# Optimization experiments

Hardware: AMD Instinct MI355X
Metric: run time of the kernel (lower is better)

## Reference

```python
import jax, jax.numpy as jnp
import numpy as np

N, E, M = 100000, 3200000, 1000000  # nodes, message edges, scored move edges
DIN, H = 128, 64


def setup_inputs() -> dict:
    key = jax.random.key(0)
    ks = jax.random.split(key, 20)
    rn = lambda k, shape, s=0.05: (jax.random.normal(k, shape, jnp.float32) * s)
    return {
        "x": jax.random.normal(ks[0], (N, DIN), jnp.float32),
        "edge_index": jax.random.randint(ks[1], (2, E), 0, N, jnp.int64),
        "move_edge_index": jax.random.randint(ks[2], (2, M), 0, N, jnp.int64),
        "lin1_w": rn(ks[3], (DIN, H)), "lin1_b": jnp.zeros((H,), jnp.float32),
        "lin2_w": rn(ks[4], (H, H)), "lin2_b": jnp.zeros((H,), jnp.float32),
        "conv1_wl": rn(ks[5], (H, H)), "conv1_bl": jnp.zeros((H,), jnp.float32),
        "conv1_wr": rn(ks[6], (H, H)),
        "conv2_wl": rn(ks[7], (H, H)), "conv2_bl": jnp.zeros((H,), jnp.float32),
        "conv2_wr": rn(ks[8], (H, H)),
        "mlp_w1": rn(ks[9], (2 * H, H)), "mlp_b1": jnp.zeros((H,), jnp.float32),
        "mlp_w2": rn(ks[10], (H, 1)), "mlp_b2": jnp.zeros((1,), jnp.float32),
    }


def reference(x, edge_index, move_edge_index,
              lin1_w, lin1_b, lin2_w, lin2_b,
              conv1_wl, conv1_bl, conv1_wr,
              conv2_wl, conv2_bl, conv2_wr,
              mlp_w1, mlp_b1, mlp_w2, mlp_b2):
    n = x.shape[0]
    src, dst = edge_index[0], edge_index[1]
    # mean-aggregation degrees (PyG SAGEConv default aggr='mean'; isolated nodes -> 0)
    deg = jax.ops.segment_sum(jnp.ones(src.shape, x.dtype), dst, num_segments=n)
    inv_deg = (jnp.where(deg > 0, 1.0 / jnp.maximum(deg, 1.0), 0.0))[:, None]

    def sage(h, wl, bl, wr):
        # out = W_l @ mean_j h_j + b_l + W_r @ h_i
        agg = jax.ops.segment_sum(h[src], dst, num_segments=n) * inv_deg
        return agg @ wl + bl + h @ wr

    h = jax.nn.relu(x @ lin1_w + lin1_b)
    h = jax.nn.relu(sage(h, conv1_wl, conv1_bl, conv1_wr))
    h = jax.nn.relu(h @ lin2_w + lin2_b)
    h = jax.nn.relu(sage(h, conv2_wl, conv2_bl, conv2_wr))

    # edge scoring: gather src/dst embeddings, concat, 2-layer MLP, tanh
    cat = jnp.concatenate([h[move_edge_index[0]], h[move_edge_index[1]]], axis=1)  # [M, 2H]
    logits = (jax.nn.relu(cat @ mlp_w1 + mlp_b1) @ mlp_w2 + mlp_b2).reshape(-1)
    return jnp.tanh(logits)
```

## Files before the change

### kernel.cpp

```cpp
#include <hip/hip_runtime.h>
#include <math.h>

#define MAXB 512
#define PART_BS 1024
#define NBLK_MAX 248
#define CAPB 96

typedef _Float16 f16;
typedef __attribute__((ext_vector_type(2))) _Float16 f16x2;
typedef __attribute__((ext_vector_type(4))) _Float16 f16x4;
typedef __attribute__((ext_vector_type(8))) _Float16 f16x8;
typedef __attribute__((ext_vector_type(4))) float f32x4;

static __device__ __forceinline__ unsigned short f2h(float f) {
    f16 h = (f16)f; return *(unsigned short*)&h;
}

__global__ __launch_bounds__(PART_BS) void k_part(const int* __restrict__ src,
                                                  const int* __restrict__ dst,
                                                  unsigned* __restrict__ bb,
                                                  int* __restrict__ cnt,
                                                  int E, int shift, int pcap,
                                                  int nblk, int nb) {
    __shared__ int h[MAXB];
    const int blk = blockIdx.x;
    const int b0 = blk * pcap;
    const int e1 = min(b0 + pcap, E);
    for (int i = threadIdx.x; i < MAXB; i += PART_BS) h[i] = 0;
    __syncthreads();
    const unsigned mask = (1u << shift) - 1u;
    for (int pos = b0 + (int)threadIdx.x * 8; pos < e1; pos += PART_BS * 8) {
        if (pos + 8 <= e1) {
            int4 d0 = *(const int4*)(dst + pos), d1 = *(const int4*)(dst + pos + 4);
            int4 s0 = *(const int4*)(src + pos), s1 = *(const int4*)(src + pos + 4);
            int dd[8] = {d0.x, d0.y, d0.z, d0.w, d1.x, d1.y, d1.z, d1.w};
            int ss[8] = {s0.x, s0.y, s0.z, s0.w, s1.x, s1.y, s1.z, s1.w};
#pragma unroll
            for (int k = 0; k < 8; ++k) {
                int b = dd[k] >> shift;
                int r = atomicAdd(&h[b], 1);
                if (r < CAPB)
                    bb[((size_t)b * nblk + blk) * CAPB + r] =
                        ((unsigned)ss[k] << shift) | ((unsigned)dd[k] & mask);
            }
        } else {
            for (int k = 0; pos + k < e1; ++k) {
                int d = dst[pos + k];
                int b = d >> shift;
                int r = atomicAdd(&h[b], 1);
                if (r < CAPB)
                    bb[((size_t)b * nblk + blk) * CAPB + r] =
                        ((unsigned)src[pos + k] << shift) | ((unsigned)d & mask);
            }
        }
    }
    __syncthreads();
    for (int i = threadIdx.x; i < nb; i += PART_BS)
        cnt[(size_t)i * nblk + blk] = min(h[i], CAPB);
}

__global__ __launch_bounds__(512) void k_bfill(const unsigned* __restrict__ bb,
                                               const int* __restrict__ cnt,
                                               int* __restrict__ row_st,
                                               int* __restrict__ row_en,
                                               float* __restrict__ inv_deg,
                                               int* __restrict__ csr,
                                               int N, int shift, int CAP, int nblk) {
    __shared__ int deg[512], cur[512], s[512];
    __shared__ int scnt[NBLK_MAX];
    int b = blockIdx.x;
    int t = threadIdx.x;
    int lo = b << shift;
    int hi = min(N, (b + 1) << shift);
    int nn = hi - lo;
    unsigned off = (unsigned)b * CAP;
    unsigned mask = (1u << shift) - 1u;
    const unsigned* seg = bb + (size_t)b * nblk * CAPB;

    for (int i = t; i < nblk; i += 512) scnt[i] = cnt[(size_t)b * nblk + i];
    deg[t] = 0;
    __syncthreads();
    const int tot8 = (nblk * CAPB) >> 3;
    for (int q8 = t; q8 < tot8; q8 += 512) {
        int i = q8 << 3;
        int si = i / CAPB;
        int r = i - si * CAPB;
        int sc = scnt[si];
        if (r < sc) {
            uint4 wA = *(const uint4*)&seg[i];
            uint4 wB = *(const uint4*)&seg[i + 4];
            int nv = min(sc - r, 8);
            unsigned ww[8] = {wA.x, wA.y, wA.z, wA.w, wB.x, wB.y, wB.z, wB.w};
#pragma unroll
            for (int k = 0; k < 8; ++k)
                if (k < nv) atomicAdd(&deg[ww[k] & mask], 1);
        }
    }
    __syncthreads();
    int d = deg[t];
    int pd = (d + 31) & ~31;
    s[t] = pd;
    __syncthreads();
    for (int o = 1; o < 512; o <<= 1) {
        int u = (t >= o) ? s[t - o] : 0;
        __syncthreads();
        s[t] += u;
        __syncthreads();
    }
    int excl = min(s[t] - pd, CAP);
    int pe = min(excl + pd, CAP);
    cur[t] = excl;
    if (t < nn) {
        row_st[lo + t] = (int)off + excl;
        row_en[lo + t] = (int)off + pe;
        inv_deg[lo + t] = d > 0 ? 1.0f / (float)d : 0.0f;
        for (int j = excl + d; j < pe; ++j) csr[off + j] = N;
    }
    __syncthreads();
    for (int q8 = t; q8 < tot8; q8 += 512) {
        int i = q8 << 3;
        int si = i / CAPB;
        int r = i - si * CAPB;
        int sc = scnt[si];
        if (r < sc) {
            uint4 wA = *(const uint4*)&seg[i];
            uint4 wB = *(const uint4*)&seg[i + 4];
            int nv = min(sc - r, 8);
            unsigned ww[8] = {wA.x, wA.y, wA.z, wA.w, wB.x, wB.y, wB.z, wB.w};
#pragma unroll
            for (int k = 0; k < 8; ++k)
                if (k < nv) {
                    int dl = (int)(ww[k] & mask);
                    int pos = atomicAdd(&cur[dl], 1);
                    if (pos < CAP) csr[off + pos] = (int)(ww[k] >> shift);
                }
        }
    }
}

__global__ __launch_bounds__(256) void k_prep(
    const float* __restrict__ lin1_w, const float* __restrict__ c1_wl,
    const float* __restrict__ c1_wr, const float* __restrict__ lin2_w,
    const float* __restrict__ c2_wl, const float* __restrict__ c2_wr,
    const float* __restrict__ mlp_w1, const float* __restrict__ mlp_w2,
    unsigned short* __restrict__ Wt) {
    int i = blockIdx.x * 256 + threadIdx.x;
    for (; i < 36928; i += gridDim.x * 256) {
        float v;
        if (i < 8192)       { int j = i;         int n = j >> 7, k = j & 127; v = lin1_w[k * 64 + n]; }
        else if (i < 16384) { int j = i - 8192;  int n = j >> 7, k = j & 127;
                              v = (k < 64) ? c1_wl[k * 64 + n] : c1_wr[(k - 64) * 64 + n]; }
        else if (i < 20480) { int j = i - 16384; int n = j >> 6, k = j & 63;  v = lin2_w[k * 64 + n]; }
        else if (i < 28672) { int j = i - 20480; int n = j >> 7, k = j & 127;
                              v = (k < 64) ? c2_wl[k * 64 + n] : c2_wr[(k - 64) * 64 + n]; }
        else if (i < 32768) { int j = i - 28672; int n = j >> 6, k = j & 63;  v = mlp_w1[k * 64 + n]; }
        else if (i < 36864) { int j = i - 32768; int n = j >> 6, k = j & 63;  v = mlp_w1[(k + 64) * 64 + n]; }
        else                { v = mlp_w2[i - 36864]; }
        Wt[i] = f2h(v);
    }
}

__global__ __launch_bounds__(256) void k_gather_h(
    const _Float16* __restrict__ hh, const int* __restrict__ csr,
    const int* __restrict__ row_st, const int* __restrict__ row_en,
    const float* __restrict__ inv_deg, _Float16* __restrict__ out, int n) {
    int node = (blockIdx.x * 256 + (int)threadIdx.x) >> 6;
    if (node >= n) return;
    int lane = threadIdx.x & 63;
    int g = lane >> 3, sub = lane & 7;
    int base = row_st[node], end = row_en[node];
    float a[8] = {0.f, 0.f, 0.f, 0.f, 0.f, 0.f, 0.f, 0.f};
#if __has_builtin(__builtin_amdgcn_fdot2)
    const f16x2 one2 = {(f16)1.f, (f16)1.f};
#endif
    for (; base + 64 <= end; base += 64) {
        int4 sA = *(const int4*)&csr[base + 4 * g];
        int4 sB = *(const int4*)&csr[base + 32 + 4 * g];
        int sidx[8] = {sA.x, sA.y, sA.z, sA.w, sB.x, sB.y, sB.z, sB.w};
        f16x8 u[8];
#pragma unroll
        for (int t = 0; t < 8; ++t)
            u[t] = *(const f16x8*)(hh + (((unsigned)sidx[t] << 6) + ((unsigned)sub << 3)));
#if __has_builtin(__builtin_amdgcn_fdot2)
#pragma unroll
        for (int t = 0; t < 8; t += 2)
#pragma unroll
            for (int j = 0; j < 8; ++j) {
                f16x2 v = {u[t][j], u[t + 1][j]};
                a[j] = __builtin_amdgcn_fdot2(v, one2, a[j], false);
            }
#else
#pragma unroll
        for (int t = 0; t < 8; ++t)
#pragma unroll
            for (int j = 0; j < 8; ++j) a[j] += (float)u[t][j];
#endif
    }
    if (base < end) {
        int4 sA = *(const int4*)&csr[base + 4 * g];
        int sidx[4] = {sA.x, sA.y, sA.z, sA.w};
        f16x8 u[4];
#pragma unroll
        for (int t = 0; t < 4; ++t)
            u[t] = *(const f16x8*)(hh + (((unsigned)sidx[t] << 6) + ((unsigned)sub << 3)));
#if __has_builtin(__builtin_amdgcn_fdot2)
#pragma unroll
        for (int t = 0; t < 4; t += 2)
#pragma unroll
            for (int j = 0; j < 8; ++j) {
                f16x2 v = {u[t][j], u[t + 1][j]};
                a[j] = __builtin_amdgcn_fdot2(v, one2, a[j], false);
            }
#else
#pragma unroll
        for (int t = 0; t < 4; ++t)
#pragma unroll
            for (int j = 0; j < 8; ++j) a[j] += (float)u[t][j];
#endif
    }
#pragma unroll
    for (int j = 0; j < 8; ++j) {
        a[j] += __shfl_xor(a[j], 8, 64);
        a[j] += __shfl_xor(a[j], 16, 64);
        a[j] += __shfl_xor(a[j], 32, 64);
    }
    if (g == 0) {
        float idv = inv_deg[node];
        f16x8 o;
#pragma unroll
        for (int j = 0; j < 8; ++j) o[j] = (f16)(a[j] * idv);
        *(f16x8*)(out + (((unsigned)node << 6) + ((unsigned)sub << 3))) = o;
    }
}

__global__ __launch_bounds__(256) void k_mm1(
    const float* __restrict__ x, const unsigned short* __restrict__ Wtg,
    const float* __restrict__ bias, unsigned short* __restrict__ outh, int n) {
    __shared__ alignas(16) unsigned short sW[64 * 136];
    const int tid = threadIdx.x;
    const int row0 = blockIdx.x * 64;
    if (blockIdx.x == 0 && tid < 8)
        ((uint4*)(outh + (size_t)n * 64))[tid] = (uint4){0, 0, 0, 0};
    for (int i = tid; i < 64 * 16; i += 256) {
        int nn = i >> 4, c = i & 15;
        *(uint4*)&sW[(nn * 17 + c) * 8] = *(const uint4*)&Wtg[i * 8];
    }
    __syncthreads();
    const int lane = tid & 63, w = tid >> 6;
    const int m = lane & 15, q = lane >> 4;
    const int gr = min(row0 + 16 * w + m, n - 1);
    const float* ar = x + (size_t)gr * 128;
    f32x4 acc[4];
#pragma unroll
    for (int c = 0; c < 4; ++c) acc[c] = (f32x4){0.f, 0.f, 0.f, 0.f};
#pragma unroll
    for (int kk = 0; kk < 4; ++kk) {
        float4 a0 = *(const float4*)(ar + kk * 32 + q * 8);
        float4 a1 = *(const float4*)(ar + kk * 32 + q * 8 + 4);
        f16x8 af;
        af[0] = (f16)a0.x; af[1] = (f16)a0.y; af[2] = (f16)a0.z; af[3] = (f16)a0.w;
        af[4] = (f16)a1.x; af[5] = (f16)a1.y; af[6] = (f16)a1.z; af[7] = (f16)a1.w;
#pragma unroll
        for (int c = 0; c < 4; ++c) {
            f16x8 bf = *(const f16x8*)&sW[((16 * c + m) * 17 + (kk * 4 + q)) * 8];
            acc[c] = __builtin_amdgcn_mfma_f32_16x16x32_f16(af, bf, acc[c], 0, 0, 0);
        }
    }
#pragma unroll
    for (int c = 0; c < 4; ++c) {
        int col = 16 * c + m;
        float bv = bias[col];
#pragma unroll
        for (int i = 0; i < 4; ++i) {
            int r = row0 + 16 * w + q * 4 + i;
            if (r < n) outh[(size_t)r * 64 + col] = f2h(fmaxf(acc[c][i] + bv, 0.f));
        }
    }
}

__global__ __launch_bounds__(256) void k_mm23(
    const unsigned short* __restrict__ aggH, const unsigned short* __restrict__ h1,
    const unsigned short* __restrict__ Wcg, const float* __restrict__ bl,
    const unsigned short* __restrict__ Wl2g, const float* __restrict__ b2,
    unsigned short* __restrict__ outh, int n) {
    __shared__ alignas(16) unsigned short sm[64 * 72 + 64 * 136];
    unsigned short* hA = sm;
    unsigned short* sW = sm + 64 * 72;
    const int tid = threadIdx.x;
    const int row0 = blockIdx.x * 64;
    for (int i = tid; i < 64 * 16; i += 256) {
        int nn = i >> 4, c = i & 15;
        *(uint4*)&sW[(nn * 17 + c) * 8] = *(const uint4*)&Wcg[i * 8];
    }
    __syncthreads();
    const int lane = tid & 63, w = tid >> 6;
    const int m = lane & 15, q = lane >> 4;
    const int gr = min(row0 + 16 * w + m, n - 1);
    f32x4 acc[4];
#pragma unroll
    for (int c = 0; c < 4; ++c) acc[c] = (f32x4){0.f, 0.f, 0.f, 0.f};
#pragma unroll
    for (int kk = 0; kk < 4; ++kk) {
        const unsigned short* ap = (kk < 2)
            ? (aggH + (size_t)gr * 64 + kk * 32 + q * 8)
            : (h1 + (size_t)gr * 64 + (kk - 2) * 32 + q * 8);
        f16x8 af = *(const f16x8*)ap;
#pragma unroll
        for (int c = 0; c < 4; ++c) {
            f16x8 bf = *(const f16x8*)&sW[((16 * c + m) * 17 + (kk * 4 + q)) * 8];
            acc[c] = __builtin_amdgcn_mfma_f32_16x16x32_f16(af, bf, acc[c], 0, 0, 0);
        }
    }
#pragma unroll
    for (int c = 0; c < 4; ++c) {
        int col = 16 * c + m;
        float bv = bl[col];
#pragma unroll
        for (int i = 0; i < 4; ++i)
            hA[(16 * w + q * 4 + i) * 72 + col] = f2h(fmaxf(acc[c][i] + bv, 0.f));
    }
    __syncthreads();
    for (int i = tid; i < 64 * 8; i += 256) {
        int nn = i >> 3, c = i & 7;
        *(uint4*)&sW[(nn * 9 + c) * 8] = *(const uint4*)&Wl2g[i * 8];
    }
    __syncthreads();
    f32x4 acc2[4];
#pragma unroll
    for (int c = 0; c < 4; ++c) acc2[c] = (f32x4){0.f, 0.f, 0.f, 0.f};
#pragma unroll
    for (int kk = 0; kk < 2; ++kk) {
        f16x8 af = *(const f16x8*)&hA[(16 * w + m) * 72 + kk * 32 + q * 8];
#pragma unroll
        for (int c = 0; c < 4; ++c) {
            f16x8 bf = *(const f16x8*)&sW[((16 * c + m) * 9 + (kk * 4 + q)) * 8];
            acc2[c] = __builtin_amdgcn_mfma_f32_16x16x32_f16(af, bf, acc2[c], 0, 0, 0);
        }
    }
#pragma unroll
    for (int c = 0; c < 4; ++c) {
        int col = 16 * c + m;
        float bv = b2[col];
#pragma unroll
        for (int i = 0; i < 4; ++i) {
            int r = row0 + 16 * w + q * 4 + i;
            if (r < n) outh[(size_t)r * 64 + col] = f2h(fmaxf(acc2[c][i] + bv, 0.f));
        }
    }
}

__global__ __launch_bounds__(256) void k_mm456(
    const unsigned short* __restrict__ aggH, const unsigned short* __restrict__ h3,
    const unsigned short* __restrict__ Wcg, const float* __restrict__ bl,
    const unsigned short* __restrict__ Wpg, const unsigned short* __restrict__ Wqg,
    const float* __restrict__ b1, unsigned short* __restrict__ Ph,
    unsigned short* __restrict__ Qh, int n) {
    __shared__ alignas(16) unsigned short sm[64 * 72 + 2 * 64 * 72];
    unsigned short* hA = sm;
    unsigned short* sW = sm + 64 * 72;
    const int tid = threadIdx.x;
    const int row0 = blockIdx.x * 64;
    for (int i = tid; i < 64 * 16; i += 256) {
        int nn = i >> 4, c = i & 15;
        *(uint4*)&sW[(nn * 17 + c) * 8] = *(const uint4*)&Wcg[i * 8];
    }
    __syncthreads();
    const int lane = tid & 63, w = tid >> 6;
    const int m = lane & 15, q = lane >> 4;
    const int gr = min(row0 + 16 * w + m, n - 1);
    f32x4 acc[4];
#pragma unroll
    for (int c = 0; c < 4; ++c) acc[c] = (f32x4){0.f, 0.f, 0.f, 0.f};
#pragma unroll
    for (int kk = 0; kk < 4; ++kk) {
        const unsigned short* ap = (kk < 2)
            ? (aggH + (size_t)gr * 64 + kk * 32 + q * 8)
            : (h3 + (size_t)gr * 64 + (kk - 2) * 32 + q * 8);
        f16x8 af = *(const f16x8*)ap;
#pragma unroll
        for (int c = 0; c < 4; ++c) {
            f16x8 bf = *(const f16x8*)&sW[((16 * c + m) * 17 + (kk * 4 + q)) * 8];
            acc[c] = __builtin_amdgcn_mfma_f32_16x16x32_f16(af, bf, acc[c], 0, 0, 0);
        }
    }
#pragma unroll
    for (int c = 0; c < 4; ++c) {
        int col = 16 * c + m;
        float bv = bl[col];
#pragma unroll
        for (int i = 0; i < 4; ++i)
            hA[(16 * w + q * 4 + i) * 72 + col] = f2h(fmaxf(acc[c][i] + bv, 0.f));
    }
    __syncthreads();
    for (int i = tid; i < 64 * 8; i += 256) {
        int nn = i >> 3, c = i & 7;
        *(uint4*)&sW[(nn * 9 + c) * 8] = *(const uint4*)&Wpg[i * 8];
        *(uint4*)&sW[4608 + (nn * 9 + c) * 8] = *(const uint4*)&Wqg[i * 8];
    }
    __syncthreads();
    f32x4 accP[4], accQ[4];
#pragma unroll
    for (int c = 0; c < 4; ++c) {
        accP[c] = (f32x4){0.f, 0.f, 0.f, 0.f};
        accQ[c] = (f32x4){0.f, 0.f, 0.f, 0.f};
    }
#pragma unroll
    for (int kk = 0; kk < 2; ++kk) {
        f16x8 af = *(const f16x8*)&hA[(16 * w + m) * 72 + kk * 32 + q * 8];
#pragma unroll
        for (int c = 0; c < 4; ++c) {
            f16x8 bp = *(const f16x8*)&sW[((16 * c + m) * 9 + (kk * 4 + q)) * 8];
            f16x8 bq = *(const f16x8*)&sW[4608 + ((16 * c + m) * 9 + (kk * 4 + q)) * 8];
            accP[c] = __builtin_amdgcn_mfma_f32_16x16x32_f16(af, bp, accP[c], 0, 0, 0);
            accQ[c] = __builtin_amdgcn_mfma_f32_16x16x32_f16(af, bq, accQ[c], 0, 0, 0);
        }
    }
#pragma unroll
    for (int c = 0; c < 4; ++c) {
        int col = 16 * c + m;
        float bv = b1[col];
#pragma unroll
        for (int i = 0; i < 4; ++i) {
            int r = row0 + 16 * w + q * 4 + i;
            if (r < n) {
                Ph[(size_t)r * 64 + col] = f2h(accP[c][i] + bv);
                Qh[(size_t)r * 64 + col] = f2h(accQ[c][i]);
            }
        }
    }
}

__global__ __launch_bounds__(256) void k_score_h(
    const _Float16* __restrict__ P, const _Float16* __restrict__ Q,
    const int* __restrict__ msrc, const int* __restrict__ mdst,
    const _Float16* __restrict__ w2h, const float* __restrict__ b2,
    float* __restrict__ out, int M) {
    int gid = blockIdx.x * 256 + threadIdx.x;
    int e = gid >> 3;
    if (e >= M) return;
    int l = gid & 7;
    int s = msrc[e], d = mdst[e];
    f16x8 p = *(const f16x8*)(P + (((unsigned)s << 6) + ((unsigned)l << 3)));
    f16x8 q = *(const f16x8*)(Q + (((unsigned)d << 6) + ((unsigned)l << 3)));
    f16x8 w = *(const f16x8*)(w2h + ((unsigned)l << 3));
    f16x8 u = p + q;
    f16x8 z = {(f16)0, (f16)0, (f16)0, (f16)0, (f16)0, (f16)0, (f16)0, (f16)0};
    u = __builtin_elementwise_max(u, z);
    float partial;
#if __has_builtin(__builtin_amdgcn_fdot2)
    f16x2 u01 = {u[0], u[1]}, u23 = {u[2], u[3]}, u45 = {u[4], u[5]}, u67 = {u[6], u[7]};
    f16x2 w01 = {w[0], w[1]}, w23 = {w[2], w[3]}, w45 = {w[4], w[5]}, w67 = {w[6], w[7]};
    partial = __builtin_amdgcn_fdot2(u01, w01,
              __builtin_amdgcn_fdot2(u23, w23,
              __builtin_amdgcn_fdot2(u45, w45,
              __builtin_amdgcn_fdot2(u67, w67, 0.f, false), false), false), false);
#else
    partial = 0.f;
#pragma unroll
    for (int i = 0; i < 8; ++i) partial += (float)u[i] * (float)w[i];
#endif
    partial += __shfl_xor(partial, 1, 8);
    partial += __shfl_xor(partial, 2, 8);
    partial += __shfl_xor(partial, 4, 8);
    if (l == 0) {
        float xx = partial + b2[0];
        float t = __expf(2.f * xx);
        out[e] = (t - 1.f) / (t + 1.f);
    }
}

extern "C" void kernel_launch(void* const* d_in, const int* in_sizes, int n_in,
                              void* d_out, int out_size, void* d_ws, size_t ws_size,
                              hipStream_t stream) {
    const float* x      = (const float*)d_in[0];
    const int*   ei     = (const int*)d_in[1];
    const int*   mei    = (const int*)d_in[2];
    const float* lin1_w = (const float*)d_in[3];
    const float* lin1_b = (const float*)d_in[4];
    const float* lin2_w = (const float*)d_in[5];
    const float* lin2_b = (const float*)d_in[6];
    const float* c1_wl  = (const float*)d_in[7];
    const float* c1_bl  = (const float*)d_in[8];
    const float* c1_wr  = (const float*)d_in[9];
    const float* c2_wl  = (const float*)d_in[10];
    const float* c2_bl  = (const float*)d_in[11];
    const float* c2_wr  = (const float*)d_in[12];
    const float* mlp_w1 = (const float*)d_in[13];
    const float* mlp_b1 = (const float*)d_in[14];
    const float* mlp_w2 = (const float*)d_in[15];
    const float* mlp_b2 = (const float*)d_in[16];

    const int N = in_sizes[0] / 128;
    const int E = in_sizes[1] / 2;
    const int M = in_sizes[2] / 2;
    const int* src  = ei;
    const int* dstE = ei + E;
    const int* msrc = mei;
    const int* mdst = mei + M;

    int shift = 8;
    while ((((N - 1) >> shift) + 1) > MAXB) ++shift;
    const int nbuckets = ((N - 1) >> shift) + 1;
    long long avg = (((long long)E << shift) / N) + 1;
    int CAP = (int)((2 * avg + 2047) & ~1023LL);

    const size_t N64 = (size_t)N * 64;
    const size_t aliasBytes = (3 * N64 + 64) * 2;
    int nblk = NBLK_MAX;
    while (nblk > 1 && (size_t)nblk * nbuckets * CAPB * 4 > aliasBytes) --nblk;
    int pcap = (((E + nblk - 1) / nblk) + 7) & ~7;
    nblk = (E + pcap - 1) / pcap;

    unsigned short* Hh   = (unsigned short*)d_ws;
    unsigned short* aggH = Hh + N64 + 64;
    unsigned short* Qh   = aggH + N64;
    float* inv_deg = (float*)(Qh + N64);
    int*   row_st  = (int*)(inv_deg + N);
    int*   row_en  = row_st + N;
    int*   cnt     = row_en + N;
    unsigned short* Wt = (unsigned short*)(cnt + (size_t)nbuckets * NBLK_MAX);
    int*   csr     = (int*)(Wt + 36928 + 32);
    unsigned* bb   = (unsigned*)Hh;
    float* outf = (float*)d_out;

    const int nbN = (N + 63) / 64;
    const int nbM = (int)(((long long)M * 8 + 255) / 256);
    const int nbG = (int)(((long long)N * 64 + 255) / 256);

    k_prep<<<64, 256, 0, stream>>>(lin1_w, c1_wl, c1_wr, lin2_w, c2_wl, c2_wr,
                                   mlp_w1, mlp_w2, Wt);
    k_part<<<nblk, PART_BS, 0, stream>>>(src, dstE, bb, cnt, E, shift, pcap,
                                         nblk, nbuckets);
    k_bfill<<<nbuckets, 512, 0, stream>>>(bb, cnt, row_st, row_en,
                                          inv_deg, csr, N, shift, CAP, nblk);

    k_mm1<<<nbN, 256, 0, stream>>>(x, Wt + 0, lin1_b, Hh, N);

    k_gather_h<<<nbG, 256, 0, stream>>>((const _Float16*)Hh, csr, row_st, row_en,
                                        inv_deg, (_Float16*)aggH, N);
    k_mm23<<<nbN, 256, 0, stream>>>(aggH, Hh, Wt + 8192, c1_bl,
                                    Wt + 16384, lin2_b, Hh, N);

    k_gather_h<<<nbG, 256, 0, stream>>>((const _Float16*)Hh, csr, row_st, row_en,
                                        inv_deg, (_Float16*)aggH, N);
    k_mm456<<<nbN, 256, 0, stream>>>(aggH, Hh, Wt + 20480, c2_bl,
                                     Wt + 28672, Wt + 32768, mlp_b1,
                                     Hh, Qh, N);

    k_score_h<<<nbM, 256, 0, stream>>>((const _Float16*)Hh, (const _Float16*)Qh,
                                       msrc, mdst, (const _Float16*)(Wt + 36864),
                                       mlp_b2, outf, M);
}
```

Before: 367.4 us.

## Fuse weight prep into partition kernel and merge bucket fill with first matmul

Removes two kernel launches. Weight transposition and fp16 conversion now run inside block 0 of the partition kernel, and the bucket-fill CSR build and the first linear layer share one heterogeneous grid so they can overlap. The partition scratch buffer is moved from Hh to aggH so the first matmul can write Hh while bucket fill still reads its data. The alias size budget changes to match. The matmul blocks now cover 128 rows with 512 threads. Block 0 of the partition kernel becomes slower because it also does the weight conversion, which could stretch that kernel's tail.

```diff
diff --git a/kernel.cpp b/kernel.cpp
--- a/kernel.cpp
+++ b/kernel.cpp
@@ -16,14 +16,32 @@
     f16 h = (f16)f; return *(unsigned short*)&h;
 }
 
-__global__ __launch_bounds__(PART_BS) void k_part(const int* __restrict__ src,
-                                                  const int* __restrict__ dst,
-                                                  unsigned* __restrict__ bb,
-                                                  int* __restrict__ cnt,
-                                                  int E, int shift, int pcap,
-                                                  int nblk, int nb) {
+__global__ __launch_bounds__(PART_BS) void k_part(
+    const int* __restrict__ src, const int* __restrict__ dst,
+    unsigned* __restrict__ bb, int* __restrict__ cnt,
+    const float* __restrict__ lin1_w, const float* __restrict__ c1_wl,
+    const float* __restrict__ c1_wr, const float* __restrict__ lin2_w,
+    const float* __restrict__ c2_wl, const float* __restrict__ c2_wr,
+    const float* __restrict__ mlp_w1, const float* __restrict__ mlp_w2,
+    unsigned short* __restrict__ Wt,
+    int E, int shift, int pcap, int nblk, int nb) {
     __shared__ int h[MAXB];
     const int blk = blockIdx.x;
+    if (blk == 0) {
+        for (int i = threadIdx.x; i < 36928; i += PART_BS) {
+            float v;
+            if (i < 8192)       { int j = i;         int n = j >> 7, k = j & 127; v = lin1_w[k * 64 + n]; }
+            else if (i < 16384) { int j = i - 8192;  int n = j >> 7, k = j & 127;
+                                  v = (k < 64) ? c1_wl[k * 64 + n] : c1_wr[(k - 64) * 64 + n]; }
+            else if (i < 20480) { int j = i - 16384; int n = j >> 6, k = j & 63;  v = lin2_w[k * 64 + n]; }
+            else if (i < 28672) { int j = i - 20480; int n = j >> 7, k = j & 127;
+                                  v = (k < 64) ? c2_wl[k * 64 + n] : c2_wr[(k - 64) * 64 + n]; }
+            else if (i < 32768) { int j = i - 28672; int n = j >> 6, k = j & 63;  v = mlp_w1[k * 64 + n]; }
+            else if (i < 36864) { int j = i - 32768; int n = j >> 6, k = j & 63;  v = mlp_w1[(k + 64) * 64 + n]; }
+            else                { v = mlp_w2[i - 36864]; }
+            Wt[i] = f2h(v);
+        }
+    }
     const int b0 = blk * pcap;
     const int e1 = min(b0 + pcap, E);
     for (int i = threadIdx.x; i < MAXB; i += PART_BS) h[i] = 0;
@@ -59,104 +77,130 @@
         cnt[(size_t)i * nblk + blk] = min(h[i], CAPB);
 }
 
-__global__ __launch_bounds__(512) void k_bfill(const unsigned* __restrict__ bb,
-                                               const int* __restrict__ cnt,
-                                               int* __restrict__ row_st,
-                                               int* __restrict__ row_en,
-                                               float* __restrict__ inv_deg,
-                                               int* __restrict__ csr,
-                                               int N, int shift, int CAP, int nblk) {
-    __shared__ int deg[512], cur[512], s[512];
-    __shared__ int scnt[NBLK_MAX];
-    int b = blockIdx.x;
-    int t = threadIdx.x;
-    int lo = b << shift;
-    int hi = min(N, (b + 1) << shift);
-    int nn = hi - lo;
-    unsigned off = (unsigned)b * CAP;
-    unsigned mask = (1u << shift) - 1u;
-    const unsigned* seg = bb + (size_t)b * nblk * CAPB;
-
-    for (int i = t; i < nblk; i += 512) scnt[i] = cnt[(size_t)b * nblk + i];
-    deg[t] = 0;
-    __syncthreads();
-    const int tot8 = (nblk * CAPB) >> 3;
-    for (int q8 = t; q8 < tot8; q8 += 512) {
-        int i = q8 << 3;
-        int si = i / CAPB;
-        int r = i - si * CAPB;
-        int sc = scnt[si];
-        if (r < sc) {
-            uint4 wA = *(const uint4*)&seg[i];
-            uint4 wB = *(const uint4*)&seg[i + 4];
-            int nv = min(sc - r, 8);
-            unsigned ww[8] = {wA.x, wA.y, wA.z, wA.w, wB.x, wB.y, wB.z, wB.w};
-#pragma unroll
-            for (int k = 0; k < 8; ++k)
-                if (k < nv) atomicAdd(&deg[ww[k] & mask], 1);
-        }
-    }
-    __syncthreads();
-    int d = deg[t];
-    int pd = (d + 31) & ~31;
-    s[t] = pd;
-    __syncthreads();
-    for (int o = 1; o < 512; o <<= 1) {
-        int u = (t >= o) ? s[t - o] : 0;
+__global__ __launch_bounds__(512) void k_bfmm(
+    const unsigned* __restrict__ bb, const int* __restrict__ cnt,
+    int* __restrict__ row_st, int* __restrict__ row_en,
+    float* __restrict__ inv_deg, int* __restrict__ csr,
+    int N, int shift, int CAP, int nblk, int nbB,
+    const float* __restrict__ x, const unsigned short* __restrict__ Wtg,
+    const float* __restrict__ bias, unsigned short* __restrict__ outh) {
+    __shared__ alignas(16) unsigned char smem[64 * 136 * 2];
+    const int t = threadIdx.x;
+
+    if (blockIdx.x < (unsigned)nbB) {
+        int* deg  = (int*)smem;
+        int* cur  = deg + 512;
+        int* s    = cur + 512;
+        int* scnt = s + 512;
+        int b = blockIdx.x;
+        int lo = b << shift;
+        int hi = min(N, (b + 1) << shift);
+        int nn = hi - lo;
+        unsigned off = (unsigned)b * CAP;
+        unsigned mask = (1u << shift) - 1u;
+        const unsigned* seg = bb + (size_t)b * nblk * CAPB;
+
+        for (int i = t; i < nblk; i += 512) scnt[i] = cnt[(size_t)b * nblk + i];
+        deg[t] = 0;
         __syncthreads();
-        s[t] += u;
+        const int tot8 = (nblk * CAPB) >> 3;
+        for (int q8 = t; q8 < tot8; q8 += 512) {
+            int i = q8 << 3;
+            int si = i / CAPB;
+            int r = i - si * CAPB;
+            int sc = scnt[si];
+            if (r < sc) {
+                uint4 wA = *(const uint4*)&seg[i];
+                uint4 wB = *(const uint4*)&seg[i + 4];
+                int nv = min(sc - r, 8);
+                unsigned ww[8] = {wA.x, wA.y, wA.z, wA.w, wB.x, wB.y, wB.z, wB.w};
+#pragma unroll
+                for (int k = 0; k < 8; ++k)
+                    if (k < nv) atomicAdd(&deg[ww[k] & mask], 1);
+            }
+        }
         __syncthreads();
-    }
-    int excl = min(s[t] - pd, CAP);
-    int pe = min(excl + pd, CAP);
-    cur[t] = excl;
-    if (t < nn) {
-        row_st[lo + t] = (int)off + excl;
-        row_en[lo + t] = (int)off + pe;
-        inv_deg[lo + t] = d > 0 ? 1.0f / (float)d : 0.0f;
-        for (int j = excl + d; j < pe; ++j) csr[off + j] = N;
-    }
-    __syncthreads();
-    for (int q8 = t; q8 < tot8; q8 += 512) {
-        int i = q8 << 3;
-        int si = i / CAPB;
-        int r = i - si * CAPB;
-        int sc = scnt[si];
-        if (r < sc) {
-            uint4 wA = *(const uint4*)&seg[i];
-            uint4 wB = *(const uint4*)&seg[i + 4];
-            int nv = min(sc - r, 8);
-            unsigned ww[8] = {wA.x, wA.y, wA.z, wA.w, wB.x, wB.y, wB.z, wB.w};
-#pragma unroll
-            for (int k = 0; k < 8; ++k)
-                if (k < nv) {
-                    int dl = (int)(ww[k] & mask);
-                    int pos = atomicAdd(&cur[dl], 1);
-                    if (pos < CAP) csr[off + pos] = (int)(ww[k] >> shift);
-                }
-        }
-    }
-}
-
-__global__ __launch_bounds__(256) void k_prep(
-    const float* __restrict__ lin1_w, const float* __restrict__ c1_wl,
-    const float* __restrict__ c1_wr, const float* __restrict__ lin2_w,
-    const float* __restrict__ c2_wl, const float* __restrict__ c2_wr,
-    const float* __restrict__ mlp_w1, const float* __restrict__ mlp_w2,
-    unsigned short* __restrict__ Wt) {
-    int i = blockIdx.x * 256 + threadIdx.x;
-    for (; i < 36928; i += gridDim.x * 256) {
-        float v;
-        if (i < 8192)       { int j = i;         int n = j >> 7, k = j & 127; v = lin1_w[k * 64 + n]; }
-        else if (i < 16384) { int j = i - 8192;  int n = j >> 7, k = j & 127;
-                              v = (k < 64) ? c1_wl[k * 64 + n] : c1_wr[(k - 64) * 64 + n]; }
-        else if (i < 20480) { int j = i - 16384; int n = j >> 6, k = j & 63;  v = lin2_w[k * 64 + n]; }
-        else if (i < 28672) { int j = i - 20480; int n = j >> 7, k = j & 127;
-                              v = (k < 64) ? c2_wl[k * 64 + n] : c2_wr[(k - 64) * 64 + n]; }
-        else if (i < 32768) { int j = i - 28672; int n = j >> 6, k = j & 63;  v = mlp_w1[k * 64 + n]; }
-        else if (i < 36864) { int j = i - 32768; int n = j >> 6, k = j & 63;  v = mlp_w1[(k + 64) * 64 + n]; }
-        else                { v = mlp_w2[i - 36864]; }
-        Wt[i] = f2h(v);
+        int d = deg[t];
+        int pd = (d + 31) & ~31;
+        s[t] = pd;
+        __syncthreads();
+        for (int o = 1; o < 512; o <<= 1) {
+            int u = (t >= o) ? s[t - o] : 0;
+            __syncthreads();
+            s[t] += u;
+            __syncthreads();
+        }
+        int excl = min(s[t] - pd, CAP);
+        int pe = min(excl + pd, CAP);
+        cur[t] = excl;
+        if (t < nn) {
+            row_st[lo + t] = (int)off + excl;
+            row_en[lo + t] = (int)off + pe;
+            inv_deg[lo + t] = d > 0 ? 1.0f / (float)d : 0.0f;
+            for (int j = excl + d; j < pe; ++j) csr[off + j] = N;
+        }
+        __syncthreads();
+        for (int q8 = t; q8 < tot8; q8 += 512) {
+            int i = q8 << 3;
+            int si = i / CAPB;
+            int r = i - si * CAPB;
+            int sc = scnt[si];
+            if (r < sc) {
+                uint4 wA = *(const uint4*)&seg[i];
+                uint4 wB = *(const uint4*)&seg[i + 4];
+                int nv = min(sc - r, 8);
+                unsigned ww[8] = {wA.x, wA.y, wA.z, wA.w, wB.x, wB.y, wB.z, wB.w};
+#pragma unroll
+                for (int k = 0; k < 8; ++k)
+                    if (k < nv) {
+                        int dl = (int)(ww[k] & mask);
+                        int pos = atomicAdd(&cur[dl], 1);
+                        if (pos < CAP) csr[off + pos] = (int)(ww[k] >> shift);
+                    }
+            }
+        }
+    } else {
+        unsigned short* sW = (unsigned short*)smem;
+        const int mb = blockIdx.x - nbB;
+        const int row0 = mb * 128;
+        const int n = N;
+        if (mb == 0 && t < 8)
+            ((uint4*)(outh + (size_t)n * 64))[t] = (uint4){0, 0, 0, 0};
+        for (int i = t; i < 64 * 16; i += 512) {
+            int nn = i >> 4, c = i & 15;
+            *(uint4*)&sW[(nn * 17 + c) * 8] = *(const uint4*)&Wtg[i * 8];
+        }
+        __syncthreads();
+        const int lane = t & 63, w = t >> 6;
+        const int m = lane & 15, q = lane >> 4;
+        const int gr = min(row0 + 16 * w + m, n - 1);
+        const float* ar = x + (size_t)gr * 128;
+        f32x4 acc[4];
+#pragma unroll
+        for (int c = 0; c < 4; ++c) acc[c] = (f32x4){0.f, 0.f, 0.f, 0.f};
+#pragma unroll
+        for (int kk = 0; kk < 4; ++kk) {
+            float4 a0 = *(const float4*)(ar + kk * 32 + q * 8);
+            float4 a1 = *(const float4*)(ar + kk * 32 + q * 8 + 4);
+            f16x8 af;
+            af[0] = (f16)a0.x; af[1] = (f16)a0.y; af[2] = (f16)a0.z; af[3] = (f16)a0.w;
+            af[4] = (f16)a1.x; af[5] = (f16)a1.y; af[6] = (f16)a1.z; af[7] = (f16)a1.w;
+#pragma unroll
+            for (int c = 0; c < 4; ++c) {
+                f16x8 bf = *(const f16x8*)&sW[((16 * c + m) * 17 + (kk * 4 + q)) * 8];
+                acc[c] = __builtin_amdgcn_mfma_f32_16x16x32_f16(af, bf, acc[c], 0, 0, 0);
+            }
+        }
+#pragma unroll
+        for (int c = 0; c < 4; ++c) {
+            int col = 16 * c + m;
+            float bv = bias[col];
+#pragma unroll
+            for (int i = 0; i < 4; ++i) {
+                int r = row0 + 16 * w + q * 4 + i;
+                if (r < n) outh[(size_t)r * 64 + col] = f2h(fmaxf(acc[c][i] + bv, 0.f));
+            }
+        }
     }
 }
 
@@ -230,51 +274,6 @@
 #pragma unroll
         for (int j = 0; j < 8; ++j) o[j] = (f16)(a[j] * idv);
         *(f16x8*)(out + (((unsigned)node << 6) + ((unsigned)sub << 3))) = o;
-    }
-}
-
-__global__ __launch_bounds__(256) void k_mm1(
-    const float* __restrict__ x, const unsigned short* __restrict__ Wtg,
-    const float* __restrict__ bias, unsigned short* __restrict__ outh, int n) {
-    __shared__ alignas(16) unsigned short sW[64 * 136];
-    const int tid = threadIdx.x;
-    const int row0 = blockIdx.x * 64;
-    if (blockIdx.x == 0 && tid < 8)
-        ((uint4*)(outh + (size_t)n * 64))[tid] = (uint4){0, 0, 0, 0};
-    for (int i = tid; i < 64 * 16; i += 256) {
-        int nn = i >> 4, c = i & 15;
-        *(uint4*)&sW[(nn * 17 + c) * 8] = *(const uint4*)&Wtg[i * 8];
-    }
-    __syncthreads();
-    const int lane = tid & 63, w = tid >> 6;
-    const int m = lane & 15, q = lane >> 4;
-    const int gr = min(row0 + 16 * w + m, n - 1);
-    const float* ar = x + (size_t)gr * 128;
-    f32x4 acc[4];
-#pragma unroll
-    for (int c = 0; c < 4; ++c) acc[c] = (f32x4){0.f, 0.f, 0.f, 0.f};
-#pragma unroll
-    for (int kk = 0; kk < 4; ++kk) {
-        float4 a0 = *(const float4*)(ar + kk * 32 + q * 8);
-        float4 a1 = *(const float4*)(ar + kk * 32 + q * 8 + 4);
-        f16x8 af;
-        af[0] = (f16)a0.x; af[1] = (f16)a0.y; af[2] = (f16)a0.z; af[3] = (f16)a0.w;
-        af[4] = (f16)a1.x; af[5] = (f16)a1.y; af[6] = (f16)a1.z; af[7] = (f16)a1.w;
-#pragma unroll
-        for (int c = 0; c < 4; ++c) {
-            f16x8 bf = *(const f16x8*)&sW[((16 * c + m) * 17 + (kk * 4 + q)) * 8];
-            acc[c] = __builtin_amdgcn_mfma_f32_16x16x32_f16(af, bf, acc[c], 0, 0, 0);
-        }
-    }
-#pragma unroll
-    for (int c = 0; c < 4; ++c) {
-        int col = 16 * c + m;
-        float bv = bias[col];
-#pragma unroll
-        for (int i = 0; i < 4; ++i) {
-            int r = row0 + 16 * w + q * 4 + i;
-            if (r < n) outh[(size_t)r * 64 + col] = f2h(fmaxf(acc[c][i] + bv, 0.f));
-        }
     }
 }
 
@@ -505,7 +504,7 @@
     int CAP = (int)((2 * avg + 2047) & ~1023LL);
 
     const size_t N64 = (size_t)N * 64;
-    const size_t aliasBytes = (3 * N64 + 64) * 2;
+    const size_t aliasBytes = (size_t)4 * N64;
     int nblk = NBLK_MAX;
     while (nblk > 1 && (size_t)nblk * nbuckets * CAPB * 4 > aliasBytes) --nblk;
     int pcap = (((E + nblk - 1) / nblk) + 7) & ~7;
@@ -520,21 +519,23 @@
     int*   cnt     = row_en + N;
     unsigned short* Wt = (unsigned short*)(cnt + (size_t)nbuckets * NBLK_MAX);
     int*   csr     = (int*)(Wt + 36928 + 32);
-    unsigned* bb   = (unsigned*)Hh;
+    unsigned* bb   = (unsigned*)aggH;
     float* outf = (float*)d_out;
 
     const int nbN = (N + 63) / 64;
+    const int nbM1 = (N + 127) / 128;
     const int nbM = (int)(((long long)M * 8 + 255) / 256);
     const int nbG = (int)(((long long)N * 64 + 255) / 256);
 
-    k_prep<<<64, 256, 0, stream>>>(lin1_w, c1_wl, c1_wr, lin2_w, c2_wl, c2_wr,
-                                   mlp_w1, mlp_w2, Wt);
-    k_part<<<nblk, PART_BS, 0, stream>>>(src, dstE, bb, cnt, E, shift, pcap,
-                                         nblk, nbuckets);
-    k_bfill<<<nbuckets, 512, 0, stream>>>(bb, cnt, row_st, row_en,
-                                          inv_deg, csr, N, shift, CAP, nblk);
-
-    k_mm1<<<nbN, 256, 0, stream>>>(x, Wt + 0, lin1_b, Hh, N);
+    k_part<<<nblk, PART_BS, 0, stream>>>(src, dstE, bb, cnt,
+                                         lin1_w, c1_wl, c1_wr, lin2_w,
+                                         c2_wl, c2_wr, mlp_w1, mlp_w2, Wt,
+                                         E, shift, pcap, nblk, nbuckets);
+
+    k_bfmm<<<nbuckets + nbM1, 512, 0, stream>>>(bb, cnt, row_st, row_en,
+                                                inv_deg, csr, N, shift, CAP,
+                                                nblk, nbuckets,
+                                                x, Wt + 0, lin1_b, Hh);
 
     k_gather_h<<<nbG, 256, 0, stream>>>((const _Float16*)Hh, csr, row_st, row_en,
                                         inv_deg, (_Float16*)aggH, N);
```

Measured after the change: 367.9 us. Within noise of the previous version (+0.1%).
